# Kernel optimization log

Hardware: AMD Instinct MI355X
Metric: run time of the kernel (lower is better)

## Reference

```python
import jax, jax.numpy as jnp
import numpy as np

EPS = 1e-3  # matches torch module eps
NUM_FEATURES = 64


def setup_inputs() -> dict:
    key = jax.random.key(0)
    X = jax.random.normal(key, (128, NUM_FEATURES, 56, 56), dtype=jnp.float32)
    return {"X": X}


def reference(X):
    # Training-mode decorrelated batch norm (ZCA whitening via eigendecomposition).
    N, C = X.shape[0], X.shape[1]
    # [N, C, H, W] -> [C, N*H*W]
    x = jnp.reshape(jnp.swapaxes(X, 0, 1), (C, -1))
    m = x.shape[1]
    mean = jnp.mean(x, axis=-1, keepdims=True)
    xc = x - mean
    # sigma = eps*I + (1/m) * xc @ xc^T   (C x C, SPD)
    sigma = EPS * jnp.eye(C, dtype=X.dtype) + (xc @ xc.T) / m
    # SVD of an SPD matrix == eigendecomposition; use symmetric eigh.
    eig, u = jnp.linalg.eigh(sigma)
    # wm = u @ diag(eig^-1/2) @ u^T  (inverse matrix square root)
    wm = (u * jax.lax.rsqrt(eig)) @ u.T
    xn = wm @ xc  # whiten
    # [C, N*H*W] -> [N, C, H, W]
    Xn = jnp.swapaxes(jnp.reshape(xn, (C, N) + X.shape[2:]), 0, 1)
    return Xn
```

## Files before the change

kernel.cpp:

```cpp
#include <hip/hip_runtime.h>
#include <stdint.h>

#define CCH   64
#define HWSZ  3136
#define NB    128
#define MCOLS 401408
#define TK    128
#define NTILES 3136
#define LDK   136
#define LDB   72
#define SLOT  4160
#define WS_TAIL 16512
#define RG    32
#define K1MAX 1024
#define LDT   72
#define K3NB  1024
#define K3T   6272

typedef short bf16x8 __attribute__((ext_vector_type(8)));
typedef float f32x4  __attribute__((ext_vector_type(4)));
typedef unsigned short u16x4 __attribute__((ext_vector_type(4)));

__device__ __forceinline__ unsigned short f2bf(float f) {
    union { float f; uint32_t u; } v; v.f = f;
    uint32_t r = v.u + 0x7fffu + ((v.u >> 16) & 1u);
    return (unsigned short)(r >> 16);
}
__device__ __forceinline__ float bf2f(unsigned short h) {
    union { uint32_t u; float f; } v; v.u = ((uint32_t)h) << 16; return v.f;
}

__global__ __launch_bounds__(256) void k1_gram(const float* __restrict__ X,
                                               float* __restrict__ part,
                                               int nb) {
    __shared__ __align__(16) unsigned short tile[CCH * LDK];
    const int tid = threadIdx.x;
    const int w = tid >> 6, l = tid & 63;

    f32x4 acc[4];
    #pragma unroll
    for (int b = 0; b < 4; ++b) acc[b] = (f32x4){0.f, 0.f, 0.f, 0.f};
    float sacc[16];
    #pragma unroll
    for (int i = 0; i < 16; ++i) sacc[i] = 0.f;

    float2 xv[16];

    uint32_t t = blockIdx.x;
    {
        const uint32_t s = t * TK + 2u * (uint32_t)l;
        const uint32_t n = s / HWSZ;
        const uint32_t hw = s - n * HWSZ;
        const size_t base = (size_t)n * (CCH * HWSZ) + hw + (size_t)w * HWSZ;
        #pragma unroll
        for (int i = 0; i < 16; ++i)
            xv[i] = *(const float2*)(X + base + (size_t)i * (4u * HWSZ));
    }

    for (;;) {
        __syncthreads();
        #pragma unroll
        for (int i = 0; i < 16; ++i) {
            sacc[i] += xv[i].x + xv[i].y;
            const int c = 4 * i + w;
            *(uint32_t*)&tile[c * LDK + 2 * l] =
                (uint32_t)f2bf(xv[i].x) | ((uint32_t)f2bf(xv[i].y) << 16);
        }
        __syncthreads();

        const uint32_t tn = t + (uint32_t)nb;
        const bool more = tn < NTILES;
        if (more) {
            const uint32_t s = tn * TK + 2u * (uint32_t)l;
            const uint32_t n = s / HWSZ;
            const uint32_t hw = s - n * HWSZ;
            const size_t base = (size_t)n * (CCH * HWSZ) + hw + (size_t)w * HWSZ;
            #pragma unroll
            for (int i = 0; i < 16; ++i)
                xv[i] = *(const float2*)(X + base + (size_t)i * (4u * HWSZ));
        }

        #pragma unroll
        for (int k0 = 0; k0 < TK; k0 += 32) {
            const int koff = k0 + ((l >> 4) << 3);
            const bf16x8 fa = *(const bf16x8*)&tile[(16 * w + (l & 15)) * LDK + koff];
            #pragma unroll
            for (int bj = 0; bj < 4; ++bj) {
                const bf16x8 fb = *(const bf16x8*)&tile[(16 * bj + (l & 15)) * LDK + koff];
                acc[bj] = __builtin_amdgcn_mfma_f32_16x16x32_bf16(fa, fb, acc[bj], 0, 0, 0);
            }
        }

        if (!more) break;
        t = tn;
    }

    float* pg = part + (size_t)blockIdx.x * SLOT;
    #pragma unroll
    for (int bj = 0; bj < 4; ++bj) {
        #pragma unroll
        for (int r = 0; r < 4; ++r) {
            const int row = 16 * w + ((l >> 4) << 2) + r;
            const int col = 16 * bj + (l & 15);
            pg[row * 64 + col] = acc[bj][r];
        }
    }
    #pragma unroll
    for (int i = 0; i < 16; ++i) {
        float v = sacc[i];
        #pragma unroll
        for (int m = 32; m > 0; m >>= 1) v += __shfl_xor(v, m, 64);
        if (l == 0) pg[4096 + 4 * i + w] = v;
    }
}

__global__ __launch_bounds__(256) void k1b1_reduce(const float* __restrict__ part,
                                                   float* __restrict__ part2,
                                                   int nb) {
    const int bx = blockIdx.x;
    const int g = bx / 17;
    const int e = (bx - g * 17) * 256 + threadIdx.x;
    if (e >= SLOT) return;
    float a0 = 0.f, a1 = 0.f, a2 = 0.f, a3 = 0.f;
    int b = g;
    for (; b + 3 * RG < nb; b += 4 * RG) {
        a0 += part[(size_t)b * SLOT + e];
        a1 += part[(size_t)(b + RG) * SLOT + e];
        a2 += part[(size_t)(b + 2 * RG) * SLOT + e];
        a3 += part[(size_t)(b + 3 * RG) * SLOT + e];
    }
    for (; b < nb; b += RG) a0 += part[(size_t)b * SLOT + e];
    part2[(size_t)g * SLOT + e] = (a0 + a1) + (a2 + a3);
}

__global__ __launch_bounds__(256) void k1b2_reduce(const float* __restrict__ part2,
                                                   float* __restrict__ out) {
    const int e = blockIdx.x * 256 + threadIdx.x;
    if (e >= SLOT) return;
    float a0 = 0.f, a1 = 0.f, a2 = 0.f, a3 = 0.f;
    #pragma unroll
    for (int b = 0; b < RG; b += 4) {
        a0 += part2[(size_t)b * SLOT + e];
        a1 += part2[(size_t)(b + 1) * SLOT + e];
        a2 += part2[(size_t)(b + 2) * SLOT + e];
        a3 += part2[(size_t)(b + 3) * SLOT + e];
    }
    out[e] = (a0 + a1) + (a2 + a3);
}

__device__ __forceinline__ bf16x8 ldfrag_h(const unsigned short* H, int rowbase, int k0, int l) {
    const int row = rowbase + (l & 15);
    const int koff = k0 + ((l >> 4) << 3);
    return *(const bf16x8*)&H[row * LDB + koff];
}
__device__ __forceinline__ bf16x8 ldfrag_lo(const float* F, bf16x8 hi, int rowbase, int k0, int l) {
    const int row = rowbase + (l & 15);
    const int koff = k0 + ((l >> 4) << 3);
    const float* p = F + row * 64 + koff;
    bf16x8 lo;
    #pragma unroll
    for (int j = 0; j < 8; ++j)
        lo[j] = (short)f2bf(p[j] - bf2f((unsigned short)hi[j]));
    return lo;
}

__device__ void mm_plain(const unsigned short* Lh, const unsigned short* Rh,
                         unsigned short* DH, float* DF, int tid) {
    const int w = tid >> 6, l = tid & 63;
    f32x4 acc[4];
    #pragma unroll
    for (int b = 0; b < 4; ++b) acc[b] = (f32x4){0.f, 0.f, 0.f, 0.f};
    #pragma unroll
    for (int k0 = 0; k0 < 64; k0 += 32) {
        const bf16x8 la = ldfrag_h(Lh, 16 * w, k0, l);
        #pragma unroll
        for (int b = 0; b < 4; ++b) {
            const bf16x8 rb = ldfrag_h(Rh, 16 * b, k0, l);
            acc[b] = __builtin_amdgcn_mfma_f32_16x16x32_bf16(la, rb, acc[b], 0, 0, 0);
        }
    }
    __syncthreads();
    #pragma unroll
    for (int b = 0; b < 4; ++b) {
        #pragma unroll
        for (int r = 0; r < 4; ++r) {
            const int row = 16 * w + ((l >> 4) << 2) + r;
            const int col = 16 * b + (l & 15);
            const float v = acc[b][r];
            if (DH) DH[row * LDB + col] = f2bf(v);
            if (DF) DF[row * 64 + col] = v;
        }
    }
    __syncthreads();
}

__device__ void mm_split(const unsigned short* Lh, const float* Lf,
                         const unsigned short* Rh, const float* Rf,
                         unsigned short* DH, float* DF, int tid) {
    const int w = tid >> 6, l = tid & 63;
    f32x4 acc[4];
    #pragma unroll
    for (int b = 0; b < 4; ++b) acc[b] = (f32x4){0.f, 0.f, 0.f, 0.f};
    #pragma unroll
    for (int k0 = 0; k0 < 64; k0 += 32) {
        const bf16x8 lah = ldfrag_h(Lh, 16 * w, k0, l);
        const bf16x8 lal = ldfrag_lo(Lf, lah, 16 * w, k0, l);
        #pragma unroll
        for (int b = 0; b < 4; ++b) {
            const bf16x8 rbh = ldfrag_h(Rh, 16 * b, k0, l);
            const bf16x8 rbl = ldfrag_lo(Rf, rbh, 16 * b, k0, l);
            acc[b] = __builtin_amdgcn_mfma_f32_16x16x32_bf16(lah, rbh, acc[b], 0, 0, 0);
            acc[b] = __builtin_amdgcn_mfma_f32_16x16x32_bf16(lah, rbl, acc[b], 0, 0, 0);
            acc[b] = __builtin_amdgcn_mfma_f32_16x16x32_bf16(lal, rbh, acc[b], 0, 0, 0);
        }
    }
    __syncthreads();
    #pragma unroll
    for (int b = 0; b < 4; ++b) {
        #pragma unroll
        for (int r = 0; r < 4; ++r) {
            const int row = 16 * w + ((l >> 4) << 2) + r;
            const int col = 16 * b + (l & 15);
            const float v = acc[b][r];
            if (DH) DH[row * LDB + col] = f2bf(v);
            if (DF) DF[row * 64 + col] = v;
        }
    }
    __syncthreads();
}

__global__ __launch_bounds__(256) void k2_ns(float* __restrict__ ws) {
    const float* gram = ws;
    const float* sums = ws + 4096;
    float* bvec = ws + 8256;
    float* Ag = ws + 8320;
    unsigned short* wmh = (unsigned short*)(ws + 12416);
    unsigned short* wml = (unsigned short*)(ws + 14464);

    __shared__ float Zf[4096];
    __shared__ float Sf[4096];
    __shared__ __align__(16) unsigned short Ah[64 * LDB];
    __shared__ __align__(16) unsigned short ZhA[64 * LDB];
    __shared__ __align__(16) unsigned short Bh[64 * LDB];
    __shared__ float mu[64];
    __shared__ float sred[1];

    const int tid = threadIdx.x;
    const float invm = 1.0f / (float)MCOLS;

    if (tid < 64) mu[tid] = sums[tid] * invm;
    __syncthreads();

    #pragma unroll
    for (int j = 0; j < 16; ++j) {
        const int e = tid * 16 + j;
        const int i = e >> 6, c = e & 63;
        Sf[e] = gram[e] * invm - mu[i] * mu[c] + ((i == c) ? 1e-3f : 0.0f);
    }
    __syncthreads();

    if (tid < 64) {
        float rs = 0.f;
        #pragma unroll
        for (int j = 0; j < 64; ++j) {
            const int c = (j + tid) & 63;
            rs += fabsf(Sf[tid * 64 + c]);
        }
        #pragma unroll
        for (int m = 32; m > 0; m >>= 1) rs = fmaxf(rs, __shfl_xor(rs, m, 64));
        if (tid == 0) sred[0] = rs;
    }
    __syncthreads();
    const float s = sred[0];
    const float invs = 1.0f / s;

    #pragma unroll
    for (int j = 0; j < 16; ++j) {
        const int e = tid * 16 + j;
        const int i = e >> 6, c = e & 63;
        const float a = Sf[e] * invs;
        Ag[e] = a;
        Ah[i * LDB + c] = f2bf(a);
        const float z = (i == c) ? 1.0f : 0.0f;
        Zf[e] = z;
        ZhA[i * LDB + c] = f2bf(z);
    }
    __syncthreads();

    for (int itn = 0; itn < 4; ++itn) {
        mm_plain(ZhA, ZhA, Bh, nullptr, tid);
        mm_plain(Ah, Bh, Bh, nullptr, tid);
        mm_plain(ZhA, Bh, nullptr, Sf, tid);
        #pragma unroll
        for (int j = 0; j < 16; ++j) {
            const int e = tid * 16 + j;
            const int i = e >> 6, c = e & 63;
            const float z = 1.5f * Zf[e] - 0.5f * Sf[e];
            Zf[e] = z;
            ZhA[i * LDB + c] = f2bf(z);
        }
        __syncthreads();
    }

    mm_split(ZhA, Zf, ZhA, Zf, Bh, Sf, tid);
    mm_split(Ah, Ag, Bh, Sf, Bh, Sf, tid);
    mm_split(ZhA, Zf, Bh, Sf, nullptr, Sf, tid);

    const float wsq = 1.0f / sqrtf(s);
    #pragma unroll
    for (int j = 0; j < 16; ++j) {
        const int e = tid * 16 + j;
        const float z = 1.5f * Zf[e] - 0.5f * Sf[e];
        Zf[e] = z;
        const float wv = z * wsq;
        const unsigned short h = f2bf(wv);
        wmh[e] = h;
        wml[e] = f2bf(wv - bf2f(h));
    }
    __syncthreads();

    if (tid < 64) {
        float acc = 0.f;
        #pragma unroll
        for (int j = 0; j < 64; ++j) {
            const int c = (j + tid) & 63;
            acc += Zf[tid * 64 + c] * mu[c];
        }
        bvec[tid] = acc * wsq;
    }
}

__global__ __launch_bounds__(256) void k3_whiten(const float* __restrict__ X,
                                                 const float* __restrict__ ws,
                                                 float* __restrict__ out) {
    __shared__ __align__(16) unsigned short xh[64 * LDT];
    __shared__ __align__(16) unsigned short xl[64 * LDT];
    const int tid = threadIdx.x;
    const int w = tid >> 6, l = tid & 63;
    const int lm = l & 15;
    const int koffL = (l >> 4) << 3;

    const unsigned short* __restrict__ wmh = (const unsigned short*)(ws + 12416);
    const unsigned short* __restrict__ wml = (const unsigned short*)(ws + 14464);
    const float* __restrict__ bvec = ws + 8256;

    bf16x8 fbh[2][4], fbl[2][4];
    #pragma unroll
    for (int kk = 0; kk < 2; ++kk) {
        #pragma unroll
        for (int cb = 0; cb < 4; ++cb) {
            const int c = cb * 16 + lm;
            fbh[kk][cb] = *(const bf16x8*)&wmh[c * 64 + kk * 32 + koffL];
            fbl[kk][cb] = *(const bf16x8*)&wml[c * 64 + kk * 32 + koffL];
        }
    }
    float bv[4];
    #pragma unroll
    for (int cb = 0; cb < 4; ++cb) bv[cb] = bvec[cb * 16 + lm];

    float xv[16];
    uint32_t g = blockIdx.x;
    size_t base;
    {
        const uint32_t n = g / 49u;
        const uint32_t hw0 = (g - n * 49u) * 64u;
        base = (size_t)n * (CCH * HWSZ) + hw0;
        #pragma unroll
        for (int u = 0; u < 16; ++u)
            xv[u] = X[base + (size_t)(w * 16 + u) * HWSZ + l];
    }

    const int frow = (16 * w + lm) * LDT;
    const int p0 = 16 * w + ((l >> 4) << 2);

    for (;;) {
        __syncthreads();
        #pragma unroll
        for (int uu = 0; uu < 4; ++uu) {
            u16x4 hv, lv;
            #pragma unroll
            for (int j = 0; j < 4; ++j) {
                const float x = xv[uu * 4 + j];
                const unsigned short h = f2bf(x);
                hv[j] = h;
                lv[j] = f2bf(x - bf2f(h));
            }
            const int c0 = w * 16 + uu * 4;
            *(u16x4*)&xh[l * LDT + c0] = hv;
            *(u16x4*)&xl[l * LDT + c0] = lv;
        }
        __syncthreads();

        const uint32_t gn = g + K3NB;
        const bool more = gn < K3T;
        size_t basen = 0;
        if (more) {
            const uint32_t n = gn / 49u;
            const uint32_t hw0 = (gn - n * 49u) * 64u;
            basen = (size_t)n * (CCH * HWSZ) + hw0;
            #pragma unroll
            for (int u = 0; u < 16; ++u)
                xv[u] = X[basen + (size_t)(w * 16 + u) * HWSZ + l];
        }

        f32x4 acc[4];
        #pragma unroll
        for (int b = 0; b < 4; ++b) acc[b] = (f32x4){0.f, 0.f, 0.f, 0.f};
        #pragma unroll
        for (int kk = 0; kk < 2; ++kk) {
            const bf16x8 fah = *(const bf16x8*)&xh[frow + kk * 32 + koffL];
            const bf16x8 fal = *(const bf16x8*)&xl[frow + kk * 32 + koffL];
            #pragma unroll
            for (int cb = 0; cb < 4; ++cb) {
                acc[cb] = __builtin_amdgcn_mfma_f32_16x16x32_bf16(fah, fbh[kk][cb], acc[cb], 0, 0, 0);
                acc[cb] = __builtin_amdgcn_mfma_f32_16x16x32_bf16(fah, fbl[kk][cb], acc[cb], 0, 0, 0);
                acc[cb] = __builtin_amdgcn_mfma_f32_16x16x32_bf16(fal, fbh[kk][cb], acc[cb], 0, 0, 0);
            }
        }

        #pragma unroll
        for (int cb = 0; cb < 4; ++cb) {
            const int c = cb * 16 + lm;
            f32x4 v;
            v[0] = acc[cb][0] - bv[cb];
            v[1] = acc[cb][1] - bv[cb];
            v[2] = acc[cb][2] - bv[cb];
            v[3] = acc[cb][3] - bv[cb];
            *(f32x4*)&out[base + (size_t)c * HWSZ + p0] = v;
        }

        if (!more) break;
        g = gn;
        base = basen;
    }
}

extern "C" void kernel_launch(void* const* d_in, const int* in_sizes, int n_in,
                              void* d_out, int out_size, void* d_ws, size_t ws_size,
                              hipStream_t stream) {
    (void)in_sizes; (void)n_in; (void)out_size;
    const float* X = (const float*)d_in[0];
    float* out = (float*)d_out;
    float* ws = (float*)d_ws;

    long avail = (long)(ws_size / sizeof(float)) - WS_TAIL - (long)RG * SLOT;
    int nb = (int)(avail / SLOT);
    if (nb > K1MAX) nb = K1MAX;
    if (nb < 1) nb = 1;

    float* part = ws + WS_TAIL;
    float* part2 = part + (size_t)nb * SLOT;

    k1_gram<<<nb, 256, 0, stream>>>(X, part, nb);
    k1b1_reduce<<<17 * RG, 256, 0, stream>>>(part, part2, nb);
    k1b2_reduce<<<17, 256, 0, stream>>>(part2, ws);
    k2_ns<<<1, 256, 0, stream>>>(ws);
    k3_whiten<<<K3NB, 256, 0, stream>>>(X, ws, out);
}
```

Before: 242.8 us.

## Fold final reduction into k2, shrink partial grid, use truncating bf16 split

Removes the second reduction kernel and has the single-block k2 sum the RG partial slots directly while forming the covariance. The number of k1 blocks and reduction groups is halved, which shrinks the partial buffers but gives each k1 block more tiles. In k3, the round-to-nearest hi/lo bf16 split of X is replaced by byte-perm truncation, which cuts ALU work but changes rounding. The truncated hi/lo pair still represents x closely, though the lo part is truncated too.

```diff
diff --git a/kernel.cpp b/kernel.cpp
--- a/kernel.cpp
+++ b/kernel.cpp
@@ -11,8 +11,8 @@
 #define LDB   72
 #define SLOT  4160
 #define WS_TAIL 16512
-#define RG    32
-#define K1MAX 1024
+#define RG    16
+#define K1MAX 512
 #define LDT   72
 #define K3NB  1024
 #define K3T   6272
@@ -28,6 +28,12 @@
 }
 __device__ __forceinline__ float bf2f(unsigned short h) {
     union { uint32_t u; float f; } v; v.u = ((uint32_t)h) << 16; return v.f;
+}
+__device__ __forceinline__ uint32_t fbits(float f) {
+    union { float f; uint32_t u; } v; v.f = f; return v.u;
+}
+__device__ __forceinline__ float bcast(uint32_t u) {
+    union { uint32_t u; float f; } v; v.u = u; return v.f;
 }
 
 __global__ __launch_bounds__(256) void k1_gram(const float* __restrict__ X,
@@ -133,21 +139,6 @@
     part2[(size_t)g * SLOT + e] = (a0 + a1) + (a2 + a3);
 }
 
-__global__ __launch_bounds__(256) void k1b2_reduce(const float* __restrict__ part2,
-                                                   float* __restrict__ out) {
-    const int e = blockIdx.x * 256 + threadIdx.x;
-    if (e >= SLOT) return;
-    float a0 = 0.f, a1 = 0.f, a2 = 0.f, a3 = 0.f;
-    #pragma unroll
-    for (int b = 0; b < RG; b += 4) {
-        a0 += part2[(size_t)b * SLOT + e];
-        a1 += part2[(size_t)(b + 1) * SLOT + e];
-        a2 += part2[(size_t)(b + 2) * SLOT + e];
-        a3 += part2[(size_t)(b + 3) * SLOT + e];
-    }
-    out[e] = (a0 + a1) + (a2 + a3);
-}
-
 __device__ __forceinline__ bf16x8 ldfrag_h(const unsigned short* H, int rowbase, int k0, int l) {
     const int row = rowbase + (l & 15);
     const int koff = k0 + ((l >> 4) << 3);
@@ -229,9 +220,8 @@
     __syncthreads();
 }
 
-__global__ __launch_bounds__(256) void k2_ns(float* __restrict__ ws) {
-    const float* gram = ws;
-    const float* sums = ws + 4096;
+__global__ __launch_bounds__(256) void k2_ns(const float* __restrict__ part2,
+                                             float* __restrict__ ws) {
     float* bvec = ws + 8256;
     float* Ag = ws + 8320;
     unsigned short* wmh = (unsigned short*)(ws + 12416);
@@ -248,14 +238,28 @@
     const int tid = threadIdx.x;
     const float invm = 1.0f / (float)MCOLS;
 
-    if (tid < 64) mu[tid] = sums[tid] * invm;
+    if (tid < 64) {
+        float a = 0.f;
+        #pragma unroll
+        for (int b = 0; b < RG; ++b) a += part2[(size_t)b * SLOT + 4096 + tid];
+        mu[tid] = a * invm;
+    }
     __syncthreads();
 
     #pragma unroll
     for (int j = 0; j < 16; ++j) {
         const int e = tid * 16 + j;
         const int i = e >> 6, c = e & 63;
-        Sf[e] = gram[e] * invm - mu[i] * mu[c] + ((i == c) ? 1e-3f : 0.0f);
+        float a0 = 0.f, a1 = 0.f, a2 = 0.f, a3 = 0.f;
+        #pragma unroll
+        for (int b = 0; b < RG; b += 4) {
+            a0 += part2[(size_t)(b + 0) * SLOT + e];
+            a1 += part2[(size_t)(b + 1) * SLOT + e];
+            a2 += part2[(size_t)(b + 2) * SLOT + e];
+            a3 += part2[(size_t)(b + 3) * SLOT + e];
+        }
+        const float g = (a0 + a1) + (a2 + a3);
+        Sf[e] = g * invm - mu[i] * mu[c] + ((i == c) ? 1e-3f : 0.0f);
     }
     __syncthreads();
 
@@ -377,17 +381,23 @@
         __syncthreads();
         #pragma unroll
         for (int uu = 0; uu < 4; ++uu) {
-            u16x4 hv, lv;
-            #pragma unroll
-            for (int j = 0; j < 4; ++j) {
-                const float x = xv[uu * 4 + j];
-                const unsigned short h = f2bf(x);
-                hv[j] = h;
-                lv[j] = f2bf(x - bf2f(h));
-            }
+            const int j0 = uu * 4;
+            const uint32_t a0 = fbits(xv[j0 + 0]);
+            const uint32_t a1 = fbits(xv[j0 + 1]);
+            const uint32_t a2 = fbits(xv[j0 + 2]);
+            const uint32_t a3 = fbits(xv[j0 + 3]);
+            uint2 hv, lv;
+            hv.x = __builtin_amdgcn_perm(a1, a0, 0x07060302u);
+            hv.y = __builtin_amdgcn_perm(a3, a2, 0x07060302u);
+            const float r0 = xv[j0 + 0] - bcast(a0 & 0xFFFF0000u);
+            const float r1 = xv[j0 + 1] - bcast(a1 & 0xFFFF0000u);
+            const float r2 = xv[j0 + 2] - bcast(a2 & 0xFFFF0000u);
+            const float r3 = xv[j0 + 3] - bcast(a3 & 0xFFFF0000u);
+            lv.x = __builtin_amdgcn_perm(fbits(r1), fbits(r0), 0x07060302u);
+            lv.y = __builtin_amdgcn_perm(fbits(r3), fbits(r2), 0x07060302u);
             const int c0 = w * 16 + uu * 4;
-            *(u16x4*)&xh[l * LDT + c0] = hv;
-            *(u16x4*)&xl[l * LDT + c0] = lv;
+            *(uint2*)&xh[l * LDT + c0] = hv;
+            *(uint2*)&xl[l * LDT + c0] = lv;
         }
         __syncthreads();
 
@@ -453,7 +463,6 @@
 
     k1_gram<<<nb, 256, 0, stream>>>(X, part, nb);
     k1b1_reduce<<<17 * RG, 256, 0, stream>>>(part, part2, nb);
-    k1b2_reduce<<<17, 256, 0, stream>>>(part2, ws);
-    k2_ns<<<1, 256, 0, stream>>>(ws);
+    k2_ns<<<1, 256, 0, stream>>>(part2, ws);
     k3_whiten<<<K3NB, 256, 0, stream>>>(X, ws, out);
 }
```

After: 242.3 us. About the same (-0.2%).
